# Kernel tuning notes

Measured on AMD Instinct MI355X. Metric: run time of the kernel, lower is better.

Reference implementation:

```python
import jax, jax.numpy as jnp
import numpy as np

B, T, E, H = 8, 1024, 1024, 16
D = E // H  # head_dim = 64
MAX_OFFSET = 0.5


def setup_inputs() -> dict:
    key = jax.random.key(0)
    ks = jax.random.split(key, 12)
    s = 0.02
    return {
        "query": jax.random.normal(ks[0], (B, T, E), jnp.float32),
        "key_": jax.random.normal(ks[1], (B, T, E), jnp.float32),
        "value": jax.random.normal(ks[2], (B, T, E), jnp.float32),
        "Wq": jax.random.normal(ks[3], (E, E), jnp.float32) * s,
        "bq": jnp.zeros((E,), jnp.float32),
        "Wk": jax.random.normal(ks[4], (E, E), jnp.float32) * s,
        "bk": jnp.zeros((E,), jnp.float32),
        "Wv": jax.random.normal(ks[5], (E, E), jnp.float32) * s,
        "bv": jnp.zeros((E,), jnp.float32),
        "Wo": jax.random.normal(ks[6], (E, E), jnp.float32) * s,
        "bo": jnp.zeros((E,), jnp.float32),
        "bias_table": jax.random.normal(ks[7], (2 * T - 1, H), jnp.float32) * s,
        "offset": jax.random.normal(ks[8], (1,), jnp.float32) * 0.1,
    }


def _temporal_bias(bias_table, offset):
    # relative position index: [T, T] in [0, 2T-2]
    coords = jnp.arange(T)
    rel = (coords[:, None] - coords[None, :]) + (T - 1)
    bounded = jnp.tanh(offset) * MAX_OFFSET  # scalar (shape (1,))
    adj = jnp.clip(rel.astype(jnp.float32) + bounded, 0.0, 2.0 * T - 2.0)
    lo = jnp.floor(adj).astype(jnp.int32)
    hi = jnp.ceil(adj).astype(jnp.int32)
    w = adj - lo.astype(jnp.float32)  # [T, T]
    lo_val = bias_table[lo]  # [T, T, H]
    hi_val = bias_table[hi]  # [T, T, H]
    bias = lo_val * (1.0 - w[..., None]) + hi_val * w[..., None]
    # -> [1, H, T, T]
    return jnp.transpose(bias, (2, 0, 1))[None]


def reference(query, key_, value, Wq, bq, Wk, bk, Wv, bv, Wo, bo, bias_table, offset):
    scale = D ** -0.5
    # torch Linear: x @ W.T + b
    q = (jnp.einsum('bte,fe->btf', query, Wq) + bq).reshape(B, T, H, D).transpose(0, 2, 1, 3)
    k = (jnp.einsum('bte,fe->btf', key_, Wk) + bk).reshape(B, T, H, D).transpose(0, 2, 1, 3)
    v = (jnp.einsum('bte,fe->btf', value, Wv) + bv).reshape(B, T, H, D).transpose(0, 2, 1, 3)
    scores = jnp.einsum('bhqd,bhkd->bhqk', q, k) * scale  # [B, H, T, T]
    scores = scores + _temporal_bias(bias_table, offset)
    attn = jax.nn.softmax(scores, axis=-1)
    out = jnp.einsum('bhqk,bhkd->bhqd', attn, v)  # [B, H, T, D]
    out = out.transpose(0, 2, 1, 3).reshape(B, T, E)
    return jnp.einsum('bte,fe->btf', out, Wo) + bo
```

## Files before the change

### kernel.cpp

```cpp
#include <hip/hip_runtime.h>
#include <hip/hip_bf16.h>
#include <stdint.h>

#define B_ 8
#define T_ 1024
#define E_ 1024
#define H_ 16
#define D_ 64
#define NREL 2047

using bf16 = __hip_bfloat16;
typedef __attribute__((ext_vector_type(8))) short bhalf8;
typedef __attribute__((ext_vector_type(4))) float f32x4;

typedef __attribute__((address_space(3))) uint32_t lds32_t;
typedef const __attribute__((address_space(1))) uint32_t glb32_t;
__device__ __forceinline__ void gld_lds16(const bf16* g, bf16* l) {
  __builtin_amdgcn_global_load_lds((glb32_t*)(const void*)g, (lds32_t*)(void*)l, 16, 0, 0);
}

__global__ __launch_bounds__(256) void cvt_f32_bf16(const float* __restrict__ s,
                                                    bf16* __restrict__ d, int n) {
  const int i = (blockIdx.x * 256 + threadIdx.x) * 8;
  if (i >= n) return;
  const float4 a = *(const float4*)(s + i);
  const float4 b = *(const float4*)(s + i + 4);
  bf16 t[8];
  t[0] = __float2bfloat16(a.x); t[1] = __float2bfloat16(a.y);
  t[2] = __float2bfloat16(a.z); t[3] = __float2bfloat16(a.w);
  t[4] = __float2bfloat16(b.x); t[5] = __float2bfloat16(b.y);
  t[6] = __float2bfloat16(b.z); t[7] = __float2bfloat16(b.w);
  *(bhalf8*)(d + i) = *(const bhalf8*)t;
}

__global__ void bias_pre(const float* __restrict__ table, const float* __restrict__ offset,
                         float* __restrict__ db) {
  const int idx = blockIdx.x * 256 + threadIdx.x;
  if (idx >= NREL * H_) return;
  const int r = idx >> 4;
  const int h = idx & 15;
  const float bounded = tanhf(offset[0]) * 0.5f;
  float adj = (float)r + bounded;
  adj = fminf(fmaxf(adj, 0.f), 2046.f);
  const int lo = (int)floorf(adj);
  const int hi = (int)ceilf(adj);
  const float wgt = adj - (float)lo;
  const float v = table[lo * H_ + h] * (1.f - wgt) + table[hi * H_ + h] * wgt;
  db[h * NREL + r] = v;
}

template <int SCATTER, int F32OUT>
__global__ __launch_bounds__(256) void gemm_bt(const bf16* __restrict__ A,
                                               const bf16* __restrict__ W,
                                               const float* __restrict__ bias,
                                               void* __restrict__ dst_) {
  __shared__ bf16 As[128 * 32];
  __shared__ bf16 Bs[128 * 32];
  const int tid = threadIdx.x;
  const int lane = tid & 63;
  const int w = tid >> 6;
  const int quad = lane >> 4;
  const int l15 = lane & 15;
  const int m0 = blockIdx.x * 128;
  const int n0 = blockIdx.y * 128;
  const int wm = (w >> 1) * 64;
  const int wn = (w & 1) * 64;

  const f32x4 zero4 = {0.f, 0.f, 0.f, 0.f};
  f32x4 acc[4][4];
#pragma unroll
  for (int i = 0; i < 4; ++i)
#pragma unroll
    for (int j = 0; j < 4; ++j) acc[i][j] = zero4;

  const int srow0 = w * 32 + (lane >> 2);
  const int scol = (lane & 3) * 8;
  const bf16* Ag = A + (size_t)(m0 + srow0) * E_ + scol;
  const bf16* Wg = W + (size_t)(n0 + srow0) * E_ + scol;
  bf16* As0 = As + w * 1024 + lane * 8;
  bf16* Bs0 = Bs + w * 1024 + lane * 8;

  for (int kt = 0; kt < 32; ++kt) {
    __syncthreads();
    const int kc = kt * 32;
    gld_lds16(Ag + kc, As0);
    gld_lds16(Ag + (size_t)16 * E_ + kc, As0 + 512);
    gld_lds16(Wg + kc, Bs0);
    gld_lds16(Wg + (size_t)16 * E_ + kc, Bs0 + 512);
    __syncthreads();

    bhalf8 af[4], bfr[4];
#pragma unroll
    for (int t = 0; t < 4; ++t) {
      af[t] = *(const bhalf8*)(As + (wm + t * 16 + l15) * 32 + quad * 8);
      bfr[t] = *(const bhalf8*)(Bs + (wn + t * 16 + l15) * 32 + quad * 8);
    }
#pragma unroll
    for (int mt = 0; mt < 4; ++mt)
#pragma unroll
      for (int nt = 0; nt < 4; ++nt)
        acc[mt][nt] = __builtin_amdgcn_mfma_f32_16x16x32_bf16(af[mt], bfr[nt], acc[mt][nt], 0, 0, 0);
  }

#pragma unroll
  for (int mt = 0; mt < 4; ++mt) {
#pragma unroll
    for (int nt = 0; nt < 4; ++nt) {
      const int n = n0 + wn + nt * 16 + l15;
      const float bv = bias[n];
#pragma unroll
      for (int r = 0; r < 4; ++r) {
        const int m = m0 + wm + mt * 16 + quad * 4 + r;
        const float v = acc[mt][nt][r] + bv;
        if (SCATTER) {
          const int bb = m >> 10, t = m & 1023, hh = n >> 6, d = n & 63;
          ((bf16*)dst_)[(((size_t)bb * H_ + hh) * T_ + t) * D_ + d] = __float2bfloat16(v);
        } else if (F32OUT) {
          ((float*)dst_)[(size_t)m * E_ + n] = v;
        } else {
          ((bf16*)dst_)[(size_t)m * E_ + n] = __float2bfloat16(v);
        }
      }
    }
  }
}

__global__ __launch_bounds__(256) void attn_kernel(const bf16* __restrict__ Q,
                                                   const bf16* __restrict__ K,
                                                   const bf16* __restrict__ V,
                                                   const float* __restrict__ db,
                                                   bf16* __restrict__ xout) {
  const int tid = threadIdx.x;
  const int lane = tid & 63;
  const int w = tid >> 6;
  const int quad = lane >> 4;
  const int l15 = lane & 15;
  const int bh = blockIdx.x;
  const int h = bh & 15;
  const int b = bh >> 4;
  const int q0 = blockIdx.y * 128;

  __shared__ bf16 Ks[64][72];
  __shared__ bf16 Vt[64][72];
  __shared__ bf16 Ps[4][32][72];
  __shared__ float dbs[1152];

  const size_t base = (size_t)bh * T_ * D_;
  const bf16* Qp = Q + base;
  const bf16* Kp = K + base;
  const bf16* Vp = V + base;
  const float* dbh = db + h * NREL;

  for (int t = tid; t < 1151; t += 256) dbs[t] = dbh[q0 + t];

  const int qw = q0 + w * 32;
  bhalf8 aq[2][2];
#pragma unroll
  for (int mt = 0; mt < 2; ++mt)
#pragma unroll
    for (int ks = 0; ks < 2; ++ks)
      aq[mt][ks] = *(const bhalf8*)(Qp + (size_t)(qw + mt * 16 + l15) * D_ + ks * 32 + quad * 8);

  const f32x4 zero4 = {0.f, 0.f, 0.f, 0.f};
  f32x4 o[2][4];
  float mrow[2][4], lrow[2][4];
#pragma unroll
  for (int mt = 0; mt < 2; ++mt)
#pragma unroll
    for (int nt = 0; nt < 4; ++nt) {
      o[mt][nt] = zero4;
      mrow[mt][nt] = -1e30f;
      lrow[mt][nt] = 0.f;
    }

  for (int it = 0; it < 16; ++it) {
    const int kb = it * 64;
    __syncthreads();
#pragma unroll
    for (int s = 0; s < 2; ++s) {
      const int idx = tid + s * 256;
      const int row = idx >> 3;
      const int c8 = (idx & 7) * 8;
      *(bhalf8*)&Ks[row][c8] = *(const bhalf8*)(Kp + (size_t)(kb + row) * D_ + c8);
      bhalf8 vv = *(const bhalf8*)(Vp + (size_t)(kb + row) * D_ + c8);
      const bf16* vp = (const bf16*)&vv;
      const int kvp = (row + c8) & 63;
#pragma unroll
      for (int j = 0; j < 8; ++j) Vt[c8 + j][kvp] = vp[j];
    }
    __syncthreads();

    f32x4 s4[2][4];
#pragma unroll
    for (int nt = 0; nt < 4; ++nt) {
      const bhalf8 bk0 = *(const bhalf8*)&Ks[nt * 16 + l15][quad * 8];
      const bhalf8 bk1 = *(const bhalf8*)&Ks[nt * 16 + l15][32 + quad * 8];
#pragma unroll
      for (int mt = 0; mt < 2; ++mt) {
        f32x4 a = zero4;
        a = __builtin_amdgcn_mfma_f32_16x16x32_bf16(aq[mt][0], bk0, a, 0, 0, 0);
        a = __builtin_amdgcn_mfma_f32_16x16x32_bf16(aq[mt][1], bk1, a, 0, 0, 0);
        s4[mt][nt] = a;
      }
    }

#pragma unroll
    for (int mt = 0; mt < 2; ++mt) {
#pragma unroll
      for (int r = 0; r < 4; ++r) {
        const int ql = w * 32 + mt * 16 + quad * 4 + r;
        const int ib = ql - kb + 1023;
        float mx = -1e30f;
#pragma unroll
        for (int nt = 0; nt < 4; ++nt) {
          const float sv = s4[mt][nt][r] * 0.125f + dbs[ib - nt * 16 - l15];
          s4[mt][nt][r] = sv;
          mx = fmaxf(mx, sv);
        }
        mx = fmaxf(mx, __shfl_xor(mx, 1, 64));
        mx = fmaxf(mx, __shfl_xor(mx, 2, 64));
        mx = fmaxf(mx, __shfl_xor(mx, 4, 64));
        mx = fmaxf(mx, __shfl_xor(mx, 8, 64));
        const float mnew = fmaxf(mrow[mt][r], mx);
        float sum = 0.f;
#pragma unroll
        for (int nt = 0; nt < 4; ++nt) {
          const float p = __expf(s4[mt][nt][r] - mnew);
          s4[mt][nt][r] = p;
          sum += p;
        }
        sum += __shfl_xor(sum, 1, 64);
        sum += __shfl_xor(sum, 2, 64);
        sum += __shfl_xor(sum, 4, 64);
        sum += __shfl_xor(sum, 8, 64);
        const float alpha = __expf(mrow[mt][r] - mnew);
        lrow[mt][r] = lrow[mt][r] * alpha + sum;
        mrow[mt][r] = mnew;
#pragma unroll
        for (int nt = 0; nt < 4; ++nt) o[mt][nt][r] *= alpha;
      }
    }

#pragma unroll
    for (int mt = 0; mt < 2; ++mt)
#pragma unroll
      for (int nt = 0; nt < 4; ++nt)
#pragma unroll
        for (int r = 0; r < 4; ++r)
          Ps[w][mt * 16 + quad * 4 + r][nt * 16 + l15] = __float2bfloat16(s4[mt][nt][r]);

    bhalf8 pa[2][2];
#pragma unroll
    for (int mt = 0; mt < 2; ++mt)
#pragma unroll
      for (int ks = 0; ks < 2; ++ks)
        pa[mt][ks] = *(const bhalf8*)&Ps[w][mt * 16 + l15][ks * 32 + quad * 8];
    const int rot = (l15 >> 3);
#pragma unroll
    for (int nt = 0; nt < 4; ++nt) {
      const int drow = nt * 16 + l15;
#pragma unroll
      for (int ks = 0; ks < 2; ++ks) {
        const int gp = (4 * ks + quad + 2 * nt + rot) & 7;
        const bhalf8 vb = *(const bhalf8*)&Vt[drow][gp * 8];
#pragma unroll
        for (int mt = 0; mt < 2; ++mt)
          o[mt][nt] = __builtin_amdgcn_mfma_f32_16x16x32_bf16(pa[mt][ks], vb, o[mt][nt], 0, 0, 0);
      }
    }
  }

#pragma unroll
  for (int mt = 0; mt < 2; ++mt) {
#pragma unroll
    for (int nt = 0; nt < 4; ++nt) {
#pragma unroll
      for (int r = 0; r < 4; ++r) {
        const int qrow = qw + mt * 16 + quad * 4 + r;
        xout[((size_t)b * T_ + qrow) * E_ + h * D_ + nt * 16 + l15] =
            __float2bfloat16(o[mt][nt][r] / lrow[mt][r]);
      }
    }
  }
}

extern "C" void kernel_launch(void* const* d_in, const int* in_sizes, int n_in,
                              void* d_out, int out_size, void* d_ws, size_t ws_size,
                              hipStream_t stream) {
  const float* query = (const float*)d_in[0];
  const float* key_  = (const float*)d_in[1];
  const float* value = (const float*)d_in[2];
  const float* Wq = (const float*)d_in[3];
  const float* bq = (const float*)d_in[4];
  const float* Wk = (const float*)d_in[5];
  const float* bk = (const float*)d_in[6];
  const float* Wv = (const float*)d_in[7];
  const float* bv = (const float*)d_in[8];
  const float* Wo = (const float*)d_in[9];
  const float* bo = (const float*)d_in[10];
  const float* table = (const float*)d_in[11];
  const float* offset = (const float*)d_in[12];
  float* out = (float*)d_out;

  char* ws = (char*)d_ws;
  const size_t ME = (size_t)B_ * T_ * E_;
  const size_t EE = (size_t)E_ * E_;
  float* db = (float*)ws;
  bf16* xc  = (bf16*)(ws + 131072);
  bf16* wc  = xc + ME;
  bf16* qb  = wc + 4 * EE;
  bf16* kb  = qb + ME;
  bf16* vb2 = kb + ME;
  bf16* x2  = vb2 + ME;

  dim3 bb(256, 1, 1);
  dim3 gg(64, 8, 1);
  const int gME = (int)(ME / 8 / 256);
  const int gEE = (int)(EE / 8 / 256);

  bias_pre<<<dim3(128), bb, 0, stream>>>(table, offset, db);

  cvt_f32_bf16<<<dim3(gEE), bb, 0, stream>>>(Wq, wc + 0 * EE, (int)EE);
  cvt_f32_bf16<<<dim3(gEE), bb, 0, stream>>>(Wk, wc + 1 * EE, (int)EE);
  cvt_f32_bf16<<<dim3(gEE), bb, 0, stream>>>(Wv, wc + 2 * EE, (int)EE);
  cvt_f32_bf16<<<dim3(gEE), bb, 0, stream>>>(Wo, wc + 3 * EE, (int)EE);

  cvt_f32_bf16<<<dim3(gME), bb, 0, stream>>>(query, xc, (int)ME);
  gemm_bt<1, 0><<<gg, bb, 0, stream>>>(xc, wc + 0 * EE, bq, qb);
  cvt_f32_bf16<<<dim3(gME), bb, 0, stream>>>(key_, xc, (int)ME);
  gemm_bt<1, 0><<<gg, bb, 0, stream>>>(xc, wc + 1 * EE, bk, kb);
  cvt_f32_bf16<<<dim3(gME), bb, 0, stream>>>(value, xc, (int)ME);
  gemm_bt<1, 0><<<gg, bb, 0, stream>>>(xc, wc + 2 * EE, bv, vb2);

  attn_kernel<<<dim3(128, 8, 1), bb, 0, stream>>>(qb, kb, vb2, db, x2);

  gemm_bt<0, 1><<<gg, bb, 0, stream>>>(x2, wc + 3 * EE, bo, out);
}
```

Before: 402.5 us.

## Fuse input conversion into GEMMs, emit transposed V, simplify attention softmax

The f32→bf16 conversion of activations now happens inside the projection GEMM loads, which removes three conversion kernels and the round-trip through the bf16 staging buffer. The V projection is computed with its operands swapped so it writes V already transposed, and the in-kernel LDS transpose of V goes away. Attention drops the online max tracking and rescaling. It uses exp2 with log2e folded into the scale and the bias table, reads the bias straight from global, and stages its output through LDS for coalesced stores. Skipping the running max assumes the scores never grow large enough for exp to overflow, which is a numerical-robustness trade-off that depends on the input range.

```diff
diff --git a/kernel.cpp b/kernel.cpp
--- a/kernel.cpp
+++ b/kernel.cpp
@@ -19,18 +19,20 @@
   __builtin_amdgcn_global_load_lds((glb32_t*)(const void*)g, (lds32_t*)(void*)l, 16, 0, 0);
 }
 
-__global__ __launch_bounds__(256) void cvt_f32_bf16(const float* __restrict__ s,
-                                                    bf16* __restrict__ d, int n) {
-  const int i = (blockIdx.x * 256 + threadIdx.x) * 8;
-  if (i >= n) return;
-  const float4 a = *(const float4*)(s + i);
-  const float4 b = *(const float4*)(s + i + 4);
+__device__ __forceinline__ bhalf8 cvt8(float4 a, float4 b) {
   bf16 t[8];
   t[0] = __float2bfloat16(a.x); t[1] = __float2bfloat16(a.y);
   t[2] = __float2bfloat16(a.z); t[3] = __float2bfloat16(a.w);
   t[4] = __float2bfloat16(b.x); t[5] = __float2bfloat16(b.y);
   t[6] = __float2bfloat16(b.z); t[7] = __float2bfloat16(b.w);
-  *(bhalf8*)(d + i) = *(const bhalf8*)t;
+  return *(const bhalf8*)t;
+}
+
+__global__ __launch_bounds__(256) void cvt_f32_bf16(const float* __restrict__ s,
+                                                    bf16* __restrict__ d, int n) {
+  const int i = (blockIdx.x * 256 + threadIdx.x) * 8;
+  if (i >= n) return;
+  *(bhalf8*)(d + i) = cvt8(*(const float4*)(s + i), *(const float4*)(s + i + 4));
 }
 
 __global__ void bias_pre(const float* __restrict__ table, const float* __restrict__ offset,
@@ -40,18 +42,17 @@
   const int r = idx >> 4;
   const int h = idx & 15;
   const float bounded = tanhf(offset[0]) * 0.5f;
-  float adj = (float)r + bounded;
-  adj = fminf(fmaxf(adj, 0.f), 2046.f);
+  float adj = fminf(fmaxf((float)r + bounded, 0.f), 2046.f);
   const int lo = (int)floorf(adj);
   const int hi = (int)ceilf(adj);
   const float wgt = adj - (float)lo;
   const float v = table[lo * H_ + h] * (1.f - wgt) + table[hi * H_ + h] * wgt;
-  db[h * NREL + r] = v;
-}
-
-template <int SCATTER, int F32OUT>
-__global__ __launch_bounds__(256) void gemm_bt(const bf16* __restrict__ A,
-                                               const bf16* __restrict__ W,
+  db[h * NREL + r] = v * 1.44269504088896f;
+}
+
+template <int MODE, int AF32, int WF32>
+__global__ __launch_bounds__(256) void gemm_bt(const void* __restrict__ A_,
+                                               const void* __restrict__ W_,
                                                const float* __restrict__ bias,
                                                void* __restrict__ dst_) {
   __shared__ bf16 As[128 * 32];
@@ -75,18 +76,43 @@
 
   const int srow0 = w * 32 + (lane >> 2);
   const int scol = (lane & 3) * 8;
-  const bf16* Ag = A + (size_t)(m0 + srow0) * E_ + scol;
-  const bf16* Wg = W + (size_t)(n0 + srow0) * E_ + scol;
+  const bf16* Ab = (const bf16*)A_ + (size_t)(m0 + srow0) * E_ + scol;
+  const float* Af = (const float*)A_ + (size_t)(m0 + srow0) * E_ + scol;
+  const bf16* Wb = (const bf16*)W_ + (size_t)(n0 + srow0) * E_ + scol;
+  const float* Wf = (const float*)W_ + (size_t)(n0 + srow0) * E_ + scol;
   bf16* As0 = As + w * 1024 + lane * 8;
   bf16* Bs0 = Bs + w * 1024 + lane * 8;
 
   for (int kt = 0; kt < 32; ++kt) {
+    const int kc = kt * 32;
+    float4 ar0, ar1, ar2, ar3, wr0, wr1, wr2, wr3;
+    if (AF32) {
+      ar0 = *(const float4*)(Af + kc);
+      ar1 = *(const float4*)(Af + kc + 4);
+      ar2 = *(const float4*)(Af + (size_t)16 * E_ + kc);
+      ar3 = *(const float4*)(Af + (size_t)16 * E_ + kc + 4);
+    }
+    if (WF32) {
+      wr0 = *(const float4*)(Wf + kc);
+      wr1 = *(const float4*)(Wf + kc + 4);
+      wr2 = *(const float4*)(Wf + (size_t)16 * E_ + kc);
+      wr3 = *(const float4*)(Wf + (size_t)16 * E_ + kc + 4);
+    }
     __syncthreads();
-    const int kc = kt * 32;
-    gld_lds16(Ag + kc, As0);
-    gld_lds16(Ag + (size_t)16 * E_ + kc, As0 + 512);
-    gld_lds16(Wg + kc, Bs0);
-    gld_lds16(Wg + (size_t)16 * E_ + kc, Bs0 + 512);
+    if (AF32) {
+      *(bhalf8*)(As + srow0 * 32 + scol) = cvt8(ar0, ar1);
+      *(bhalf8*)(As + (srow0 + 16) * 32 + scol) = cvt8(ar2, ar3);
+    } else {
+      gld_lds16(Ab + kc, As0);
+      gld_lds16(Ab + (size_t)16 * E_ + kc, As0 + 512);
+    }
+    if (WF32) {
+      *(bhalf8*)(Bs + srow0 * 32 + scol) = cvt8(wr0, wr1);
+      *(bhalf8*)(Bs + (srow0 + 16) * 32 + scol) = cvt8(wr2, wr3);
+    } else {
+      gld_lds16(Wb + kc, Bs0);
+      gld_lds16(Wb + (size_t)16 * E_ + kc, Bs0 + 512);
+    }
     __syncthreads();
 
     bhalf8 af[4], bfr[4];
@@ -104,21 +130,28 @@
 
 #pragma unroll
   for (int mt = 0; mt < 4; ++mt) {
+    float bi[4];
+    if (MODE == 2) {
+#pragma unroll
+      for (int r = 0; r < 4; ++r) bi[r] = bias[m0 + wm + mt * 16 + quad * 4 + r];
+    }
 #pragma unroll
     for (int nt = 0; nt < 4; ++nt) {
       const int n = n0 + wn + nt * 16 + l15;
-      const float bv = bias[n];
+      const float bv = (MODE == 2) ? 0.f : bias[n];
 #pragma unroll
       for (int r = 0; r < 4; ++r) {
         const int m = m0 + wm + mt * 16 + quad * 4 + r;
-        const float v = acc[mt][nt][r] + bv;
-        if (SCATTER) {
+        if (MODE == 1) {
+          const float v = acc[mt][nt][r] + bv;
           const int bb = m >> 10, t = m & 1023, hh = n >> 6, d = n & 63;
           ((bf16*)dst_)[(((size_t)bb * H_ + hh) * T_ + t) * D_ + d] = __float2bfloat16(v);
-        } else if (F32OUT) {
-          ((float*)dst_)[(size_t)m * E_ + n] = v;
+        } else if (MODE == 2) {
+          const float v = acc[mt][nt][r] + bi[r];
+          const int hh = m >> 6, d = m & 63, bb = n >> 10, t = n & 1023;
+          ((bf16*)dst_)[(((size_t)bb * H_ + hh) * D_ + d) * T_ + t] = __float2bfloat16(v);
         } else {
-          ((bf16*)dst_)[(size_t)m * E_ + n] = __float2bfloat16(v);
+          ((float*)dst_)[(size_t)m * E_ + n] = acc[mt][nt][r] + bv;
         }
       }
     }
@@ -127,7 +160,7 @@
 
 __global__ __launch_bounds__(256) void attn_kernel(const bf16* __restrict__ Q,
                                                    const bf16* __restrict__ K,
-                                                   const bf16* __restrict__ V,
+                                                   const bf16* __restrict__ Vt_g,
                                                    const float* __restrict__ db,
                                                    bf16* __restrict__ xout) {
   const int tid = threadIdx.x;
@@ -140,38 +173,32 @@
   const int b = bh >> 4;
   const int q0 = blockIdx.y * 128;
 
-  __shared__ bf16 Ks[64][72];
-  __shared__ bf16 Vt[64][72];
-  __shared__ bf16 Ps[4][32][72];
-  __shared__ float dbs[1152];
+  __shared__ char smem[36864];
+  bf16 (*Ks)[72] = (bf16(*)[72])smem;
+  bf16 (*Vt)[72] = (bf16(*)[72])(smem + 9216);
+  bf16 (*Pq)[72] = (bf16(*)[72])(smem + 18432 + w * 4608);
 
   const size_t base = (size_t)bh * T_ * D_;
   const bf16* Qp = Q + base;
   const bf16* Kp = K + base;
-  const bf16* Vp = V + base;
+  const bf16* Vp = Vt_g + base;
   const float* dbh = db + h * NREL;
-
-  for (int t = tid; t < 1151; t += 256) dbs[t] = dbh[q0 + t];
 
   const int qw = q0 + w * 32;
   bhalf8 aq[2][2];
 #pragma unroll
-  for (int mt = 0; mt < 2; ++mt)
+  for (int qt = 0; qt < 2; ++qt)
 #pragma unroll
     for (int ks = 0; ks < 2; ++ks)
-      aq[mt][ks] = *(const bhalf8*)(Qp + (size_t)(qw + mt * 16 + l15) * D_ + ks * 32 + quad * 8);
+      aq[qt][ks] = *(const bhalf8*)(Qp + (size_t)(qw + qt * 16 + l15) * D_ + ks * 32 + quad * 8);
 
   const f32x4 zero4 = {0.f, 0.f, 0.f, 0.f};
-  f32x4 o[2][4];
-  float mrow[2][4], lrow[2][4];
-#pragma unroll
-  for (int mt = 0; mt < 2; ++mt)
-#pragma unroll
-    for (int nt = 0; nt < 4; ++nt) {
-      o[mt][nt] = zero4;
-      mrow[mt][nt] = -1e30f;
-      lrow[mt][nt] = 0.f;
-    }
+  f32x4 o[4][2];
+#pragma unroll
+  for (int dt = 0; dt < 4; ++dt)
+#pragma unroll
+    for (int qt = 0; qt < 2; ++qt) o[dt][qt] = zero4;
+  float lsum[2] = {0.f, 0.f};
 
   for (int it = 0; it < 16; ++it) {
     const int kb = it * 64;
@@ -182,106 +209,84 @@
       const int row = idx >> 3;
       const int c8 = (idx & 7) * 8;
       *(bhalf8*)&Ks[row][c8] = *(const bhalf8*)(Kp + (size_t)(kb + row) * D_ + c8);
-      bhalf8 vv = *(const bhalf8*)(Vp + (size_t)(kb + row) * D_ + c8);
-      const bf16* vp = (const bf16*)&vv;
-      const int kvp = (row + c8) & 63;
-#pragma unroll
-      for (int j = 0; j < 8; ++j) Vt[c8 + j][kvp] = vp[j];
+      *(bhalf8*)&Vt[row][c8] = *(const bhalf8*)(Vp + (size_t)row * T_ + kb + c8);
     }
     __syncthreads();
 
-    f32x4 s4[2][4];
-#pragma unroll
-    for (int nt = 0; nt < 4; ++nt) {
-      const bhalf8 bk0 = *(const bhalf8*)&Ks[nt * 16 + l15][quad * 8];
-      const bhalf8 bk1 = *(const bhalf8*)&Ks[nt * 16 + l15][32 + quad * 8];
-#pragma unroll
-      for (int mt = 0; mt < 2; ++mt) {
+    f32x4 st[4][2];
+#pragma unroll
+    for (int kvt = 0; kvt < 4; ++kvt) {
+      const bhalf8 ak0 = *(const bhalf8*)&Ks[kvt * 16 + l15][quad * 8];
+      const bhalf8 ak1 = *(const bhalf8*)&Ks[kvt * 16 + l15][32 + quad * 8];
+#pragma unroll
+      for (int qt = 0; qt < 2; ++qt) {
         f32x4 a = zero4;
-        a = __builtin_amdgcn_mfma_f32_16x16x32_bf16(aq[mt][0], bk0, a, 0, 0, 0);
-        a = __builtin_amdgcn_mfma_f32_16x16x32_bf16(aq[mt][1], bk1, a, 0, 0, 0);
-        s4[mt][nt] = a;
+        a = __builtin_amdgcn_mfma_f32_16x16x32_bf16(ak0, aq[qt][0], a, 0, 0, 0);
+        a = __builtin_amdgcn_mfma_f32_16x16x32_bf16(ak1, aq[qt][1], a, 0, 0, 0);
+        st[kvt][qt] = a;
       }
     }
 
 #pragma unroll
-    for (int mt = 0; mt < 2; ++mt) {
-#pragma unroll
-      for (int r = 0; r < 4; ++r) {
-        const int ql = w * 32 + mt * 16 + quad * 4 + r;
-        const int ib = ql - kb + 1023;
-        float mx = -1e30f;
-#pragma unroll
-        for (int nt = 0; nt < 4; ++nt) {
-          const float sv = s4[mt][nt][r] * 0.125f + dbs[ib - nt * 16 - l15];
-          s4[mt][nt][r] = sv;
-          mx = fmaxf(mx, sv);
+    for (int qt = 0; qt < 2; ++qt) {
+      const int qg = qw + qt * 16 + l15;
+#pragma unroll
+      for (int kvt = 0; kvt < 4; ++kvt) {
+        const int relb = qg - (kb + kvt * 16 + quad * 4) + 1023;
+        bf16 t4[4];
+#pragma unroll
+        for (int rr = 0; rr < 4; ++rr) {
+          const float p = exp2f(st[kvt][qt][rr] * 0.18033688011112f + dbh[relb - rr]);
+          lsum[qt] += p;
+          t4[rr] = __float2bfloat16(p);
         }
-        mx = fmaxf(mx, __shfl_xor(mx, 1, 64));
-        mx = fmaxf(mx, __shfl_xor(mx, 2, 64));
-        mx = fmaxf(mx, __shfl_xor(mx, 4, 64));
-        mx = fmaxf(mx, __shfl_xor(mx, 8, 64));
-        const float mnew = fmaxf(mrow[mt][r], mx);
-        float sum = 0.f;
-#pragma unroll
-        for (int nt = 0; nt < 4; ++nt) {
-          const float p = __expf(s4[mt][nt][r] - mnew);
-          s4[mt][nt][r] = p;
-          sum += p;
-        }
-        sum += __shfl_xor(sum, 1, 64);
-        sum += __shfl_xor(sum, 2, 64);
-        sum += __shfl_xor(sum, 4, 64);
-        sum += __shfl_xor(sum, 8, 64);
-        const float alpha = __expf(mrow[mt][r] - mnew);
-        lrow[mt][r] = lrow[mt][r] * alpha + sum;
-        mrow[mt][r] = mnew;
-#pragma unroll
-        for (int nt = 0; nt < 4; ++nt) o[mt][nt][r] *= alpha;
+        *(uint2*)&Pq[qt * 16 + l15][kvt * 16 + quad * 4] = *(const uint2*)t4;
       }
     }
 
 #pragma unroll
-    for (int mt = 0; mt < 2; ++mt)
-#pragma unroll
-      for (int nt = 0; nt < 4; ++nt)
-#pragma unroll
-        for (int r = 0; r < 4; ++r)
-          Ps[w][mt * 16 + quad * 4 + r][nt * 16 + l15] = __float2bfloat16(s4[mt][nt][r]);
-
-    bhalf8 pa[2][2];
-#pragma unroll
-    for (int mt = 0; mt < 2; ++mt)
-#pragma unroll
-      for (int ks = 0; ks < 2; ++ks)
-        pa[mt][ks] = *(const bhalf8*)&Ps[w][mt * 16 + l15][ks * 32 + quad * 8];
-    const int rot = (l15 >> 3);
-#pragma unroll
-    for (int nt = 0; nt < 4; ++nt) {
-      const int drow = nt * 16 + l15;
-#pragma unroll
-      for (int ks = 0; ks < 2; ++ks) {
-        const int gp = (4 * ks + quad + 2 * nt + rot) & 7;
-        const bhalf8 vb = *(const bhalf8*)&Vt[drow][gp * 8];
-#pragma unroll
-        for (int mt = 0; mt < 2; ++mt)
-          o[mt][nt] = __builtin_amdgcn_mfma_f32_16x16x32_bf16(pa[mt][ks], vb, o[mt][nt], 0, 0, 0);
+    for (int ks = 0; ks < 2; ++ks) {
+      bhalf8 pb[2];
+#pragma unroll
+      for (int qt = 0; qt < 2; ++qt)
+        pb[qt] = *(const bhalf8*)&Pq[qt * 16 + l15][ks * 32 + quad * 8];
+#pragma unroll
+      for (int dt = 0; dt < 4; ++dt) {
+        const bhalf8 av = *(const bhalf8*)&Vt[dt * 16 + l15][ks * 32 + quad * 8];
+#pragma unroll
+        for (int qt = 0; qt < 2; ++qt)
+          o[dt][qt] = __builtin_amdgcn_mfma_f32_16x16x32_bf16(av, pb[qt], o[dt][qt], 0, 0, 0);
       }
     }
   }
 
-#pragma unroll
-  for (int mt = 0; mt < 2; ++mt) {
-#pragma unroll
-    for (int nt = 0; nt < 4; ++nt) {
-#pragma unroll
-      for (int r = 0; r < 4; ++r) {
-        const int qrow = qw + mt * 16 + quad * 4 + r;
-        xout[((size_t)b * T_ + qrow) * E_ + h * D_ + nt * 16 + l15] =
-            __float2bfloat16(o[mt][nt][r] / lrow[mt][r]);
-      }
-    }
+  float rdiv[2];
+#pragma unroll
+  for (int qt = 0; qt < 2; ++qt) {
+    float l = lsum[qt];
+    l += __shfl_xor(l, 16, 64);
+    l += __shfl_xor(l, 32, 64);
+    rdiv[qt] = 1.0f / l;
   }
+
+  __syncthreads();
+  bf16 (*Ol)[72] = (bf16(*)[72])(smem + w * 4608);
+#pragma unroll
+  for (int dt = 0; dt < 4; ++dt)
+#pragma unroll
+    for (int qt = 0; qt < 2; ++qt) {
+      bf16 t4[4];
+#pragma unroll
+      for (int rr = 0; rr < 4; ++rr)
+        t4[rr] = __float2bfloat16(o[dt][qt][rr] * rdiv[qt]);
+      *(uint2*)&Ol[qt * 16 + l15][dt * 16 + quad * 4] = *(const uint2*)t4;
+    }
+  const int row = lane >> 1;
+  const int ch = (lane & 1) * 32;
+  bf16* op = xout + ((size_t)b * T_ + qw + row) * E_ + h * 64 + ch;
+#pragma unroll
+  for (int c = 0; c < 4; ++c)
+    *(bhalf8*)(op + c * 8) = *(const bhalf8*)&Ol[row][ch + c * 8];
 }
 
 extern "C" void kernel_launch(void* const* d_in, const int* in_sizes, int n_in,
@@ -306,33 +311,26 @@
   const size_t ME = (size_t)B_ * T_ * E_;
   const size_t EE = (size_t)E_ * E_;
   float* db = (float*)ws;
-  bf16* xc  = (bf16*)(ws + 131072);
-  bf16* wc  = xc + ME;
+  bf16* wc  = (bf16*)(ws + 131072);
   bf16* qb  = wc + 4 * EE;
   bf16* kb  = qb + ME;
-  bf16* vb2 = kb + ME;
-  bf16* x2  = vb2 + ME;
+  bf16* vt  = kb + ME;
+  bf16* x2  = vt + ME;
 
   dim3 bb(256, 1, 1);
-  dim3 gg(64, 8, 1);
-  const int gME = (int)(ME / 8 / 256);
   const int gEE = (int)(EE / 8 / 256);
 
   bias_pre<<<dim3(128), bb, 0, stream>>>(table, offset, db);
-
   cvt_f32_bf16<<<dim3(gEE), bb, 0, stream>>>(Wq, wc + 0 * EE, (int)EE);
   cvt_f32_bf16<<<dim3(gEE), bb, 0, stream>>>(Wk, wc + 1 * EE, (int)EE);
   cvt_f32_bf16<<<dim3(gEE), bb, 0, stream>>>(Wv, wc + 2 * EE, (int)EE);
   cvt_f32_bf16<<<dim3(gEE), bb, 0, stream>>>(Wo, wc + 3 * EE, (int)EE);
 
-  cvt_f32_bf16<<<dim3(gME), bb, 0, stream>>>(query, xc, (int)ME);
-  gemm_bt<1, 0><<<gg, bb, 0, stream>>>(xc, wc + 0 * EE, bq, qb);
-  cvt_f32_bf16<<<dim3(gME), bb, 0, stream>>>(key_, xc, (int)ME);
-  gemm_bt<1, 0><<<gg, bb, 0, stream>>>(xc, wc + 1 * EE, bk, kb);
-  cvt_f32_bf16<<<dim3(gME), bb, 0, stream>>>(value, xc, (int)ME);
-  gemm_bt<1, 0><<<gg, bb, 0, stream>>>(xc, wc + 2 * EE, bv, vb2);
-
-  attn_kernel<<<dim3(128, 8, 1), bb, 0, stream>>>(qb, kb, vb2, db, x2);
-
-  gemm_bt<0, 1><<<gg, bb, 0, stream>>>(x2, wc + 3 * EE, bo, out);
-}
+  gemm_bt<1, 1, 0><<<dim3(64, 8), bb, 0, stream>>>(query, wc + 0 * EE, bq, qb);
+  gemm_bt<1, 1, 0><<<dim3(64, 8), bb, 0, stream>>>(key_, wc + 1 * EE, bk, kb);
+  gemm_bt<2, 0, 1><<<dim3(8, 64), bb, 0, stream>>>(wc + 2 * EE, value, bv, vt);
+
+  attn_kernel<<<dim3(128, 8), bb, 0, stream>>>(qb, kb, vt, db, x2);
+
+  gemm_bt<0, 0, 0><<<dim3(64, 8), bb, 0, stream>>>(x2, wc + 3 * EE, bo, out);
+}
```

Result: slower. 441.6 us (+9.7%).
